# Kernel tuning notes

Measured on AMD Instinct MI355X. Metric: run time of the kernel, lower is better.

The kernel has to match this reference:

```python
import jax, jax.numpy as jnp
import numpy as np

B, S = 2, 2048
D_MODEL, N_HEAD = 2048, 16
D_K = D_MODEL // N_HEAD        # 128
D_C, D_CQ = 512, 1024
D_ROPE = 64
D_NOPE = D_K - D_ROPE          # 64
EPS = 1.1920929e-07            # torch.finfo(float32).eps (nn.RMSNorm default)


def rms_norm(x, w):
    var = jnp.mean(x * x, axis=-1, keepdims=True)
    return x * jax.lax.rsqrt(var + EPS) * w


def setup_inputs() -> dict:
    key = jax.random.key(0)
    ks = jax.random.split(key, 16)
    g = lambda k, shape: (jax.random.normal(k, shape, dtype=jnp.float32) * 0.02)
    return {
        "x": jax.random.normal(ks[0], (B, S, D_MODEL), dtype=jnp.float32),
        "q_down_w": g(ks[1], (D_CQ, D_MODEL)),
        "q_down_b": g(ks[2], (D_CQ,)),
        "q_norm_w": jnp.ones((D_CQ,), jnp.float32),
        "q_up_w": g(ks[3], (N_HEAD * D_K, D_CQ)),
        "q_up_b": g(ks[4], (N_HEAD * D_K,)),
        "kv_down_w": g(ks[5], (D_C, D_MODEL)),
        "kv_down_b": g(ks[6], (D_C,)),
        "kv_norm_w": jnp.ones((D_C,), jnp.float32),
        "kv_up_w": g(ks[7], (N_HEAD * (D_NOPE + D_K), D_C)),
        "kv_up_b": g(ks[8], (N_HEAD * (D_NOPE + D_K),)),
        "k_rope_w": g(ks[9], (N_HEAD * D_ROPE, D_MODEL)),
        "k_rope_b": g(ks[10], (N_HEAD * D_ROPE,)),
        "out_w": g(ks[11], (D_MODEL, D_MODEL)),
        "out_b": g(ks[12], (D_MODEL,)),
    }


def reference(x, q_down_w, q_down_b, q_norm_w, q_up_w, q_up_b,
              kv_down_w, kv_down_b, kv_norm_w, kv_up_w, kv_up_b,
              k_rope_w, k_rope_b, out_w, out_b):
    b, s, _ = x.shape
    # Q low-rank path: down -> RMSNorm -> up
    c_q = rms_norm(x @ q_down_w.T + q_down_b, q_norm_w)              # [b,s,d_cq]
    q = (c_q @ q_up_w.T + q_up_b).reshape(b, s, N_HEAD, D_K)
    q = jnp.transpose(q, (0, 2, 1, 3))                               # [b,h,s,d_k]
    q_nope, q_rope = q[..., :D_NOPE], q[..., D_NOPE:]
    # KV low-rank path
    c_kv = rms_norm(x @ kv_down_w.T + kv_down_b, kv_norm_w)          # [b,s,d_c]
    kv = (c_kv @ kv_up_w.T + kv_up_b).reshape(b, s, N_HEAD, D_NOPE + D_K)
    kv = jnp.transpose(kv, (0, 2, 1, 3))                             # [b,h,s,d_nope+d_k]
    k_nope, v = kv[..., :D_NOPE], kv[..., D_NOPE:]
    # decoupled rope subspace (rope=None config: no rotation applied)
    k_rope = (x @ k_rope_w.T + k_rope_b).reshape(b, s, N_HEAD, D_ROPE)
    k_rope = jnp.transpose(k_rope, (0, 2, 1, 3))                     # [b,h,s,d_rope]
    q = jnp.concatenate([q_nope, q_rope], axis=-1)                   # [b,h,s,d_k]
    k = jnp.concatenate([k_nope, k_rope], axis=-1)                   # [b,h,s,d_k]
    # causal attention
    scores = jnp.einsum('bhnd,bhmd->bhnm', q, k) / np.sqrt(D_K).astype(np.float32)
    mask = jnp.tril(jnp.ones((s, s), dtype=bool))
    scores = jnp.where(mask, scores, -jnp.inf)
    probs = jax.nn.softmax(scores, axis=-1)
    attn = jnp.einsum('bhnm,bhmd->bhnd', probs, v)                   # [b,h,s,d_k]
    attn = jnp.transpose(attn, (0, 2, 1, 3)).reshape(b, s, D_MODEL)
    return attn @ out_w.T + out_b
```

## Files before the change

kernel.cpp:

```cpp
#include <hip/hip_runtime.h>
#include <hip/hip_bf16.h>

typedef __attribute__((ext_vector_type(8))) short bf16x8;
typedef __attribute__((ext_vector_type(4))) float f32x4;
typedef unsigned short u16;

#define RMS_EPS 1.1920929e-07f

constexpr int Bb = 2, Ss = 2048, DM = 2048, NH = 16;
constexpr int MROWS = Bb * Ss;

__device__ __forceinline__ u16 f2bf(float f) {
    __hip_bfloat16 h = __float2bfloat16(f);
    return *reinterpret_cast<u16*>(&h);
}

__device__ __forceinline__ float exp2_fast(float x) {
    float r; asm("v_exp_f32 %0, %1" : "=v"(r) : "v"(x)); return r;
}

__device__ __forceinline__ void gload16(const void* g, void* l) {
    __builtin_amdgcn_global_load_lds(
        (const __attribute__((address_space(1))) unsigned int*)g,
        (__attribute__((address_space(3))) unsigned int*)l, 16, 0, 0);
}

__global__ __launch_bounds__(256) void cvt_all(
    const float* __restrict__ s0, u16* __restrict__ d0,
    const float* __restrict__ s1, u16* __restrict__ d1,
    const float* __restrict__ s2, u16* __restrict__ d2,
    const float* __restrict__ s3, u16* __restrict__ d3,
    const float* __restrict__ s4, u16* __restrict__ d4,
    const float* __restrict__ s5, u16* __restrict__ d5,
    const float* __restrict__ s6, u16* __restrict__ d6)
{
    int i = blockIdx.x * 256 + threadIdx.x;
    const float* s; u16* d; int off;
    if (i < 2097152)      { s = s0; d = d0; off = 0; }
    else if (i < 2621440) { s = s1; d = d1; off = 2097152; }
    else if (i < 2883584) { s = s2; d = d2; off = 2621440; }
    else if (i < 3407872) { s = s3; d = d3; off = 2883584; }
    else if (i < 3932160) { s = s4; d = d4; off = 3407872; }
    else if (i < 4325376) { s = s5; d = d5; off = 3932160; }
    else                  { s = s6; d = d6; off = 4325376; }
    int j = i - off;
    float4 v = reinterpret_cast<const float4*>(s)[j];
    ushort4 o;
    o.x = f2bf(v.x); o.y = f2bf(v.y); o.z = f2bf(v.z); o.w = f2bf(v.w);
    reinterpret_cast<ushort4*>(d)[j] = o;
}

__global__ void build_bcat(const float* __restrict__ qb, const float* __restrict__ kvb,
                           const float* __restrict__ krb, float* __restrict__ bcat) {
    int i = blockIdx.x * 256 + threadIdx.x;
    if (i < 1024) bcat[i] = qb[i];
    else if (i < 1536) bcat[i] = kvb[i - 1024];
    else if (i < 2560) bcat[i] = krb[i - 1536];
}

template <typename OutT>
__global__ __launch_bounds__(256) void gemm_bt(
    const u16* __restrict__ A, const u16* __restrict__ Bt,
    const float* __restrict__ bias, OutT* __restrict__ C,
    int M, int N, int K)
{
    __shared__ alignas(16) u16 sA[128 * 32];
    __shared__ alignas(16) u16 sB[128 * 32];
    const int tid = threadIdx.x;
    const int lane = tid & 63;
    const int w = tid >> 6;
    const int wr = w >> 1, wc = w & 1;
    const int l16 = lane & 15, lq = lane >> 4;
    const int tileM = blockIdx.y * 128;
    const int tileN = blockIdx.x * 128;

    f32x4 acc[4][4];
#pragma unroll
    for (int m = 0; m < 4; m++)
#pragma unroll
        for (int n = 0; n < 4; n++)
#pragma unroll
            for (int r = 0; r < 4; r++) acc[m][n][r] = 0.f;

    const int srow = w * 16 + (lane >> 2);
    const int scol = (lane & 3) * 8;
    const u16* gA0 = A + (size_t)(tileM + srow) * K + scol;
    const u16* gA1 = A + (size_t)(tileM + srow + 64) * K + scol;
    const u16* gB0 = Bt + (size_t)(tileN + srow) * K + scol;
    const u16* gB1 = Bt + (size_t)(tileN + srow + 64) * K + scol;
    u16* lA0 = sA + w * 512;
    u16* lA1 = sA + 2048 + w * 512;
    u16* lB0 = sB + w * 512;
    u16* lB1 = sB + 2048 + w * 512;

    int aoff[4], boff[4];
#pragma unroll
    for (int m = 0; m < 4; m++) aoff[m] = (wr * 64 + m * 16 + l16) * 32 + lq * 8;
#pragma unroll
    for (int n = 0; n < 4; n++) boff[n] = (wc * 64 + n * 16 + l16) * 32 + lq * 8;

    const int nk = K >> 5;
    for (int kk = 0; kk < nk; ++kk) {
        __syncthreads();
        gload16(gA0, lA0);
        gload16(gA1, lA1);
        gload16(gB0, lB0);
        gload16(gB1, lB1);
        gA0 += 32; gA1 += 32; gB0 += 32; gB1 += 32;
        __syncthreads();
        bf16x8 af[4], bfr[4];
#pragma unroll
        for (int m = 0; m < 4; m++) af[m] = *(const bf16x8*)&sA[aoff[m]];
#pragma unroll
        for (int n = 0; n < 4; n++) bfr[n] = *(const bf16x8*)&sB[boff[n]];
        __builtin_amdgcn_s_setprio(1);
#pragma unroll
        for (int m = 0; m < 4; m++)
#pragma unroll
            for (int n = 0; n < 4; n++)
                acc[m][n] = __builtin_amdgcn_mfma_f32_16x16x32_bf16(af[m], bfr[n], acc[m][n], 0, 0, 0);
        __builtin_amdgcn_s_setprio(0);
    }

#pragma unroll
    for (int n = 0; n < 4; n++) {
        int col = tileN + wc * 64 + n * 16 + l16;
        float bv = bias ? bias[col] : 0.f;
#pragma unroll
        for (int m = 0; m < 4; m++) {
            int rowb = tileM + wr * 64 + m * 16 + (lq << 2);
#pragma unroll
            for (int r = 0; r < 4; r++) {
                float v = acc[m][n][r] + bv;
                if constexpr (sizeof(OutT) == 2)
                    C[(size_t)(rowb + r) * N + col] = (OutT)f2bf(v);
                else
                    C[(size_t)(rowb + r) * N + col] = (OutT)v;
            }
        }
    }
}

__global__ __launch_bounds__(256) void gemm_down(
    const u16* __restrict__ A, const u16* __restrict__ Bt,
    const float* __restrict__ bcat, float* __restrict__ dcat,
    u16* __restrict__ krbuf)
{
    constexpr int K = 2048;
    __shared__ alignas(16) u16 sA[128 * 32];
    __shared__ alignas(16) u16 sB[128 * 32];
    const int tid = threadIdx.x;
    const int lane = tid & 63;
    const int w = tid >> 6;
    const int wr = w >> 1, wc = w & 1;
    const int l16 = lane & 15, lq = lane >> 4;
    const int tileM = blockIdx.y * 128;
    const int tileN = blockIdx.x * 128;

    f32x4 acc[4][4];
#pragma unroll
    for (int m = 0; m < 4; m++)
#pragma unroll
        for (int n = 0; n < 4; n++)
#pragma unroll
            for (int r = 0; r < 4; r++) acc[m][n][r] = 0.f;

    const int srow = w * 16 + (lane >> 2);
    const int scol = (lane & 3) * 8;
    const u16* gA0 = A + (size_t)(tileM + srow) * K + scol;
    const u16* gA1 = A + (size_t)(tileM + srow + 64) * K + scol;
    const u16* gB0 = Bt + (size_t)(tileN + srow) * K + scol;
    const u16* gB1 = Bt + (size_t)(tileN + srow + 64) * K + scol;
    u16* lA0 = sA + w * 512;
    u16* lA1 = sA + 2048 + w * 512;
    u16* lB0 = sB + w * 512;
    u16* lB1 = sB + 2048 + w * 512;

    int aoff[4], boff[4];
#pragma unroll
    for (int m = 0; m < 4; m++) aoff[m] = (wr * 64 + m * 16 + l16) * 32 + lq * 8;
#pragma unroll
    for (int n = 0; n < 4; n++) boff[n] = (wc * 64 + n * 16 + l16) * 32 + lq * 8;

    const int nk = K >> 5;
    for (int kk = 0; kk < nk; ++kk) {
        __syncthreads();
        gload16(gA0, lA0);
        gload16(gA1, lA1);
        gload16(gB0, lB0);
        gload16(gB1, lB1);
        gA0 += 32; gA1 += 32; gB0 += 32; gB1 += 32;
        __syncthreads();
        bf16x8 af[4], bfr[4];
#pragma unroll
        for (int m = 0; m < 4; m++) af[m] = *(const bf16x8*)&sA[aoff[m]];
#pragma unroll
        for (int n = 0; n < 4; n++) bfr[n] = *(const bf16x8*)&sB[boff[n]];
        __builtin_amdgcn_s_setprio(1);
#pragma unroll
        for (int m = 0; m < 4; m++)
#pragma unroll
            for (int n = 0; n < 4; n++)
                acc[m][n] = __builtin_amdgcn_mfma_f32_16x16x32_bf16(af[m], bfr[n], acc[m][n], 0, 0, 0);
        __builtin_amdgcn_s_setprio(0);
    }

    const bool isrope = (tileN >= 1536);
#pragma unroll
    for (int n = 0; n < 4; n++) {
        int col = tileN + wc * 64 + n * 16 + l16;
        float bv = bcat[col];
#pragma unroll
        for (int m = 0; m < 4; m++) {
            int rowb = tileM + wr * 64 + m * 16 + (lq << 2);
#pragma unroll
            for (int r = 0; r < 4; r++) {
                float v = acc[m][n][r] + bv;
                if (!isrope) dcat[(size_t)(rowb + r) * 1536 + col] = v;
                else         krbuf[(size_t)(rowb + r) * 1024 + (col - 1536)] = f2bf(v);
            }
        }
    }
}

template <int C>
__global__ __launch_bounds__(256) void rmsnorm_bf16(
    const float* __restrict__ in, int istride, const float* __restrict__ wgt, u16* __restrict__ out)
{
    const int row = blockIdx.x;
    const int tid = threadIdx.x;
    constexpr int PER = C / 256;
    const float* p = in + (size_t)row * istride;
    float v[PER];
    float ss = 0.f;
#pragma unroll
    for (int i = 0; i < PER; i++) { v[i] = p[tid + i * 256]; ss += v[i] * v[i]; }
#pragma unroll
    for (int o = 32; o; o >>= 1) ss += __shfl_xor(ss, o, 64);
    __shared__ float red[4];
    if ((tid & 63) == 0) red[tid >> 6] = ss;
    __syncthreads();
    float tot = red[0] + red[1] + red[2] + red[3];
    float inv = rsqrtf(tot / (float)C + RMS_EPS);
    u16* q = out + (size_t)row * C;
#pragma unroll
    for (int i = 0; i < PER; i++) {
        int c = tid + i * 256;
        q[c] = f2bf(v[i] * inv * wgt[c]);
    }
}

__global__ __launch_bounds__(256) void transpose_v(
    const u16* __restrict__ kvbuf, u16* __restrict__ vT)
{
    __shared__ alignas(16) u16 tile[64][72];
    const int tid = threadIdx.x;
    const int t0 = blockIdx.x * 64;
    const int h = blockIdx.y >> 1, dh = blockIdx.y & 1;
    const int trow = tid >> 2, c8 = (tid & 3) * 8;
    const u16* src = kvbuf + (size_t)(t0 + trow) * 3072 + h * 192 + 64 + dh * 64 + c8;
    *(bf16x8*)&tile[trow][c8]      = *(const bf16x8*)src;
    *(bf16x8*)&tile[trow][c8 + 32] = *(const bf16x8*)(src + 32);
    __syncthreads();
    const int drow = tid >> 2, tc8 = (tid & 3) * 8;
    bf16x8 a, b2;
#pragma unroll
    for (int j = 0; j < 8; j++) {
        a[j]  = (short)tile[tc8 + j][drow];
        b2[j] = (short)tile[tc8 + 32 + j][drow];
    }
    u16* dst = vT + (size_t)(h * 128 + dh * 64 + drow) * MROWS + t0 + tc8;
    *(bf16x8*)dst = a;
    *(bf16x8*)(dst + 32) = b2;
}

__global__ __launch_bounds__(256) void mla_attn(
    const u16* __restrict__ qbuf,
    const u16* __restrict__ kvbuf,
    const u16* __restrict__ krbuf,
    const u16* __restrict__ vT,
    u16* __restrict__ obuf)
{
    const int bh = blockIdx.x;
    const int yy = blockIdx.y;
    const int ii = yy & 7, jj = yy >> 3;
    const int qt = (jj == 0) ? (ii * 2) : (jj == 1) ? (31 - ii * 2)
                 : (jj == 2) ? (ii * 2 + 1) : (30 - ii * 2);
    const int b = bh >> 4, h = bh & 15;
    const int tid = threadIdx.x, lane = tid & 63, w = tid >> 6;
    const int l16 = lane & 15, lq = lane >> 4;

    __shared__ alignas(16) u16 sK[64 * 128];
    __shared__ alignas(16) u16 sVt[128 * 64];
    __shared__ alignas(16) u16 sPT[4][16 * 64];

    const int rowbase = b * Ss;
    const int q0 = qt * 64;
    char* pbase = (char*)sPT[w];

    const int sr = tid >> 2, sc = (tid & 3) * 32;
    const int vd = tid >> 1, vh = (tid & 1) * 32;
    const float C1 = 0.12751742f;
    const float THRR = 90.5f;

    bf16x8 qf[4];
    {
        const u16* qp = qbuf + (size_t)(rowbase + q0 + w * 16 + l16) * 2048 + h * 128 + lq * 8;
#pragma unroll
        for (int c = 0; c < 4; c++) qf[c] = *(const bf16x8*)(qp + c * 32);
    }
    float mi = -3e38f, li = 0.f;
    f32x4 o[8];
#pragma unroll
    for (int d = 0; d < 8; d++)
#pragma unroll
        for (int r = 0; r < 4; r++) o[d][r] = 0.f;

    bf16x8 kr[4], vr[4];
    {
        const int krow = rowbase + sr;
        const u16* src = (sc < 64)
            ? kvbuf + (size_t)krow * 3072 + h * 192 + sc
            : krbuf + (size_t)krow * 1024 + h * 64 + (sc - 64);
#pragma unroll
        for (int j = 0; j < 4; j++) kr[j] = *(const bf16x8*)(src + j * 8);
        const u16* vsrc = vT + (size_t)(h * 128 + vd) * MROWS + rowbase + vh;
#pragma unroll
        for (int j = 0; j < 4; j++) vr[j] = *(const bf16x8*)(vsrc + j * 8);
    }

    for (int kt = 0; kt <= qt; ++kt) {
        __syncthreads();
#pragma unroll
        for (int j = 0; j < 4; j++) {
            int byteoff = sr * 256 + (sc + j * 8) * 2;
            *(bf16x8*)((char*)sK + (byteoff ^ ((sr & 7) << 4))) = kr[j];
        }
#pragma unroll
        for (int j = 0; j < 4; j++) {
            int byteoff = vd * 128 + (vh + j * 8) * 2;
            *(bf16x8*)((char*)sVt + (byteoff ^ ((vd & 7) << 4))) = vr[j];
        }
        __syncthreads();
        if (kt < qt) {
            const int krow = rowbase + (kt + 1) * 64 + sr;
            const u16* src = (sc < 64)
                ? kvbuf + (size_t)krow * 3072 + h * 192 + sc
                : krbuf + (size_t)krow * 1024 + h * 64 + (sc - 64);
#pragma unroll
            for (int j = 0; j < 4; j++) kr[j] = *(const bf16x8*)(src + j * 8);
            const u16* vsrc = vT + (size_t)(h * 128 + vd) * MROWS + rowbase + (kt + 1) * 64 + vh;
#pragma unroll
            for (int j = 0; j < 4; j++) vr[j] = *(const bf16x8*)(vsrc + j * 8);
        }

        f32x4 scf[4];
#pragma unroll
        for (int n = 0; n < 4; n++)
#pragma unroll
            for (int r = 0; r < 4; r++) scf[n][r] = 0.f;
        __builtin_amdgcn_s_setprio(1);
#pragma unroll
        for (int n = 0; n < 4; n++) {
#pragma unroll
            for (int c = 0; c < 4; c++) {
                int row = n * 16 + l16;
                int byteoff = row * 256 + (c * 32 + lq * 8) * 2;
                bf16x8 kf = *(const bf16x8*)((char*)sK + (byteoff ^ ((row & 7) << 4)));
                scf[n] = __builtin_amdgcn_mfma_f32_16x16x32_bf16(kf, qf[c], scf[n], 0, 0, 0);
            }
        }
        __builtin_amdgcn_s_setprio(0);

        if (kt == qt) {
            const int qg = w * 16 + l16;
#pragma unroll
            for (int n = 0; n < 4; n++)
#pragma unroll
                for (int r = 0; r < 4; r++) {
                    int kg = n * 16 + lq * 4 + r;
                    if (kg > qg) scf[n][r] = -3e38f;
                }
        }
        float mx = mi;
#pragma unroll
        for (int n = 0; n < 4; n++)
#pragma unroll
            for (int r = 0; r < 4; r++) mx = fmaxf(mx, scf[n][r]);
        mx = fmaxf(mx, __shfl_xor(mx, 16, 64));
        mx = fmaxf(mx, __shfl_xor(mx, 32, 64));
        if (!__all(mx - mi <= THRR)) {
            float f = exp2_fast((mi - mx) * C1);
            li *= f;
#pragma unroll
            for (int d = 0; d < 8; d++)
#pragma unroll
                for (int r = 0; r < 4; r++) o[d][r] *= f;
            mi = mx;
        }
        float mc = mi * C1;
        float rs = 0.f;
#pragma unroll
        for (int n = 0; n < 4; n++)
#pragma unroll
            for (int r = 0; r < 4; r++) {
                float pv = exp2_fast(__fmaf_rn(scf[n][r], C1, -mc));
                scf[n][r] = pv;
                rs += pv;
            }
        rs += __shfl_xor(rs, 16, 64);
        rs += __shfl_xor(rs, 32, 64);
        li += rs;

#pragma unroll
        for (int n = 0; n < 4; n++) {
            ushort4 pk;
            pk.x = f2bf(scf[n][0]); pk.y = f2bf(scf[n][1]);
            pk.z = f2bf(scf[n][2]); pk.w = f2bf(scf[n][3]);
            int byteoff = l16 * 128 + n * 32 + lq * 8;
            *(ushort4*)(pbase + (byteoff ^ ((l16 & 7) << 4))) = pk;
        }
        __builtin_amdgcn_s_setprio(1);
#pragma unroll
        for (int c = 0; c < 2; c++) {
            int pbyte = l16 * 128 + (c * 32 + lq * 8) * 2;
            bf16x8 pf = *(const bf16x8*)(pbase + (pbyte ^ ((l16 & 7) << 4)));
#pragma unroll
            for (int d = 0; d < 8; d++) {
                int vrow = d * 16 + l16;
                int vbyte = vrow * 128 + (c * 32 + lq * 8) * 2;
                bf16x8 vf = *(const bf16x8*)((char*)sVt + (vbyte ^ ((vrow & 7) << 4)));
                o[d] = __builtin_amdgcn_mfma_f32_16x16x32_bf16(vf, pf, o[d], 0, 0, 0);
            }
        }
        __builtin_amdgcn_s_setprio(0);
    }
    float invl = 1.f / li;
    u16* op = obuf + (size_t)(rowbase + q0 + w * 16 + l16) * 2048 + h * 128;
#pragma unroll
    for (int d = 0; d < 8; d++) {
        ushort4 ok;
        ok.x = f2bf(o[d][0] * invl); ok.y = f2bf(o[d][1] * invl);
        ok.z = f2bf(o[d][2] * invl); ok.w = f2bf(o[d][3] * invl);
        *(ushort4*)(op + d * 16 + lq * 4) = ok;
    }
}

extern "C" void kernel_launch(void* const* d_in, const int* in_sizes, int n_in,
                              void* d_out, int out_size, void* d_ws, size_t ws_size,
                              hipStream_t stream) {
    const float* x        = (const float*)d_in[0];
    const float* q_down_w = (const float*)d_in[1];
    const float* q_down_b = (const float*)d_in[2];
    const float* q_norm_w = (const float*)d_in[3];
    const float* q_up_w   = (const float*)d_in[4];
    const float* q_up_b   = (const float*)d_in[5];
    const float* kv_down_w= (const float*)d_in[6];
    const float* kv_down_b= (const float*)d_in[7];
    const float* kv_norm_w= (const float*)d_in[8];
    const float* kv_up_w  = (const float*)d_in[9];
    const float* kv_up_b  = (const float*)d_in[10];
    const float* k_rope_w = (const float*)d_in[11];
    const float* k_rope_b = (const float*)d_in[12];
    const float* out_w    = (const float*)d_in[13];
    const float* out_b    = (const float*)d_in[14];

    char* ws = (char*)d_ws;
    u16* xbf    = (u16*)(ws + 0);
    u16* wcat   = (u16*)(ws + 16777216);
    u16* quw    = (u16*)(ws + 27262976);
    u16* kvuw   = (u16*)(ws + 31457280);
    u16* outw   = (u16*)(ws + 34603008);
    float* bcat = (float*)(ws + 42991616);
    float* dcat = (float*)(ws + 43008000);
    u16* cq     = (u16*)(ws + 68173824);
    u16* ckv    = (u16*)(ws + 76562432);
    u16* qbuf   = (u16*)(ws + 80756736);
    u16* kvbuf  = (u16*)(ws + 97533952);
    u16* krbuf  = (u16*)(ws + 122699776);
    u16* vT     = (u16*)(ws + 0);
    u16* attnbuf= (u16*)(ws + 43008000);

    cvt_all<<<20992, 256, 0, stream>>>(
        x, xbf,
        q_down_w,  wcat,
        kv_down_w, wcat + 1024 * 2048,
        k_rope_w,  wcat + 1536 * 2048,
        q_up_w,    quw,
        kv_up_w,   kvuw,
        out_w,     outw);
    build_bcat<<<10, 256, 0, stream>>>(q_down_b, kv_down_b, k_rope_b, bcat);

    gemm_down<<<dim3(20, 32), 256, 0, stream>>>(xbf, wcat, bcat, dcat, krbuf);
    rmsnorm_bf16<1024><<<MROWS, 256, 0, stream>>>(dcat, 1536, q_norm_w, cq);
    rmsnorm_bf16<512><<<MROWS, 256, 0, stream>>>(dcat + 1024, 1536, kv_norm_w, ckv);
    gemm_bt<u16><<<dim3(16, 32), 256, 0, stream>>>(cq, quw, q_up_b, qbuf, MROWS, 2048, 1024);
    gemm_bt<u16><<<dim3(24, 32), 256, 0, stream>>>(ckv, kvuw, kv_up_b, kvbuf, MROWS, 3072, 512);
    transpose_v<<<dim3(64, 32), 256, 0, stream>>>(kvbuf, vT);
    mla_attn<<<dim3(32, 32), 256, 0, stream>>>(qbuf, kvbuf, krbuf, vT, attnbuf);
    gemm_bt<float><<<dim3(16, 32), 256, 0, stream>>>(attnbuf, outw, out_b, (float*)d_out, MROWS, 2048, 2048);
}
```

Measured before the change: 285.4 us.

## Rework attention to 128-row query tiles with 32x32 MFMA and register P

Attention blocks now cover 128 query rows, with each wave owning 32 rows. Scores and PV products use 32x32x16 bf16 MFMAs, and P is exchanged through lane shuffles instead of an LDS staging buffer. This halves the number of blocks and doubles K/V reuse per LDS load, and waves whose rows are fully masked skip compute. The GEMM kernels also get an XCD-aware block remap to improve L2 locality, and launch bounds request two blocks per CU for attention. The trade-off is higher register pressure and fewer blocks for load balance.

```diff
diff --git a/kernel.cpp b/kernel.cpp
--- a/kernel.cpp
+++ b/kernel.cpp
@@ -3,7 +3,9 @@
 
 typedef __attribute__((ext_vector_type(8))) short bf16x8;
 typedef __attribute__((ext_vector_type(4))) float f32x4;
+typedef __attribute__((ext_vector_type(16))) float f32x16;
 typedef unsigned short u16;
+typedef unsigned int u32;
 
 #define RMS_EPS 1.1920929e-07f
 
@@ -58,6 +60,17 @@
     else if (i < 2560) bcat[i] = krb[i - 1536];
 }
 
+__device__ __forceinline__ void xcd_remap(int& bx, int& by) {
+    int nx = gridDim.x, ny = gridDim.y;
+    int nwg = nx * ny;
+    if ((nwg & 7) != 0) return;
+    int flat = blockIdx.x + nx * blockIdx.y;
+    int chunk = nwg >> 3;
+    int wg = (flat & 7) * chunk + (flat >> 3);
+    by = wg % ny;
+    bx = wg / ny;
+}
+
 template <typename OutT>
 __global__ __launch_bounds__(256) void gemm_bt(
     const u16* __restrict__ A, const u16* __restrict__ Bt,
@@ -71,8 +84,10 @@
     const int w = tid >> 6;
     const int wr = w >> 1, wc = w & 1;
     const int l16 = lane & 15, lq = lane >> 4;
-    const int tileM = blockIdx.y * 128;
-    const int tileN = blockIdx.x * 128;
+    int bx = blockIdx.x, by = blockIdx.y;
+    xcd_remap(bx, by);
+    const int tileM = by * 128;
+    const int tileN = bx * 128;
 
     f32x4 acc[4][4];
 #pragma unroll
@@ -154,8 +169,10 @@
     const int w = tid >> 6;
     const int wr = w >> 1, wc = w & 1;
     const int l16 = lane & 15, lq = lane >> 4;
-    const int tileM = blockIdx.y * 128;
-    const int tileN = blockIdx.x * 128;
+    int bx = blockIdx.x, by = blockIdx.y;
+    xcd_remap(bx, by);
+    const int tileM = by * 128;
+    const int tileN = bx * 128;
 
     f32x4 acc[4][4];
 #pragma unroll
@@ -274,7 +291,7 @@
     *(bf16x8*)(dst + 32) = b2;
 }
 
-__global__ __launch_bounds__(256) void mla_attn(
+__global__ __launch_bounds__(256, 2) void mla_attn(
     const u16* __restrict__ qbuf,
     const u16* __restrict__ kvbuf,
     const u16* __restrict__ krbuf,
@@ -282,54 +299,53 @@
     u16* __restrict__ obuf)
 {
     const int bh = blockIdx.x;
-    const int yy = blockIdx.y;
-    const int ii = yy & 7, jj = yy >> 3;
-    const int qt = (jj == 0) ? (ii * 2) : (jj == 1) ? (31 - ii * 2)
-                 : (jj == 2) ? (ii * 2 + 1) : (30 - ii * 2);
-    const int b = bh >> 4, h = bh & 15;
+    const int y = blockIdx.y;
+    const int ii = y & 7, jj = y >> 3;
+    const int qt = jj ? (15 - 2 * ii) : (2 * ii);
+    const int b = bh >> 4, hh = bh & 15;
     const int tid = threadIdx.x, lane = tid & 63, w = tid >> 6;
-    const int l16 = lane & 15, lq = lane >> 4;
+    const int l31 = lane & 31, hx = lane >> 5;
 
     __shared__ alignas(16) u16 sK[64 * 128];
     __shared__ alignas(16) u16 sVt[128 * 64];
-    __shared__ alignas(16) u16 sPT[4][16 * 64];
 
     const int rowbase = b * Ss;
-    const int q0 = qt * 64;
-    char* pbase = (char*)sPT[w];
+    const int q0 = qt * 128;
+    const int nkt = 2 * qt + 2;
 
     const int sr = tid >> 2, sc = (tid & 3) * 32;
     const int vd = tid >> 1, vh = (tid & 1) * 32;
     const float C1 = 0.12751742f;
     const float THRR = 90.5f;
 
-    bf16x8 qf[4];
+    bf16x8 qf[8];
     {
-        const u16* qp = qbuf + (size_t)(rowbase + q0 + w * 16 + l16) * 2048 + h * 128 + lq * 8;
-#pragma unroll
-        for (int c = 0; c < 4; c++) qf[c] = *(const bf16x8*)(qp + c * 32);
+        const u16* qp = qbuf + (size_t)(rowbase + q0 + w * 32 + l31) * 2048 + hh * 128;
+#pragma unroll
+        for (int c = 0; c < 8; c++) qf[c] = *(const bf16x8*)(qp + (2 * c + hx) * 8);
     }
     float mi = -3e38f, li = 0.f;
-    f32x4 o[8];
-#pragma unroll
-    for (int d = 0; d < 8; d++)
-#pragma unroll
-        for (int r = 0; r < 4; r++) o[d][r] = 0.f;
+    f32x16 o[4];
+#pragma unroll
+    for (int d = 0; d < 4; d++)
+#pragma unroll
+        for (int i = 0; i < 16; i++) o[d][i] = 0.f;
 
     bf16x8 kr[4], vr[4];
     {
         const int krow = rowbase + sr;
         const u16* src = (sc < 64)
-            ? kvbuf + (size_t)krow * 3072 + h * 192 + sc
-            : krbuf + (size_t)krow * 1024 + h * 64 + (sc - 64);
+            ? kvbuf + (size_t)krow * 3072 + hh * 192 + sc
+            : krbuf + (size_t)krow * 1024 + hh * 64 + (sc - 64);
 #pragma unroll
         for (int j = 0; j < 4; j++) kr[j] = *(const bf16x8*)(src + j * 8);
-        const u16* vsrc = vT + (size_t)(h * 128 + vd) * MROWS + rowbase + vh;
+        const u16* vsrc = vT + (size_t)(hh * 128 + vd) * MROWS + rowbase + vh;
 #pragma unroll
         for (int j = 0; j < 4; j++) vr[j] = *(const bf16x8*)(vsrc + j * 8);
     }
 
-    for (int kt = 0; kt <= qt; ++kt) {
+#pragma unroll 1
+    for (int kt = 0; kt < nkt; ++kt) {
         __syncthreads();
 #pragma unroll
         for (int j = 0; j < 4; j++) {
@@ -342,108 +358,123 @@
             *(bf16x8*)((char*)sVt + (byteoff ^ ((vd & 7) << 4))) = vr[j];
         }
         __syncthreads();
-        if (kt < qt) {
+        if (kt + 1 < nkt) {
             const int krow = rowbase + (kt + 1) * 64 + sr;
             const u16* src = (sc < 64)
-                ? kvbuf + (size_t)krow * 3072 + h * 192 + sc
-                : krbuf + (size_t)krow * 1024 + h * 64 + (sc - 64);
+                ? kvbuf + (size_t)krow * 3072 + hh * 192 + sc
+                : krbuf + (size_t)krow * 1024 + hh * 64 + (sc - 64);
 #pragma unroll
             for (int j = 0; j < 4; j++) kr[j] = *(const bf16x8*)(src + j * 8);
-            const u16* vsrc = vT + (size_t)(h * 128 + vd) * MROWS + rowbase + (kt + 1) * 64 + vh;
+            const u16* vsrc = vT + (size_t)(hh * 128 + vd) * MROWS + rowbase + (kt + 1) * 64 + vh;
 #pragma unroll
             for (int j = 0; j < 4; j++) vr[j] = *(const bf16x8*)(vsrc + j * 8);
         }
 
-        f32x4 scf[4];
-#pragma unroll
-        for (int n = 0; n < 4; n++)
-#pragma unroll
-            for (int r = 0; r < 4; r++) scf[n][r] = 0.f;
-        __builtin_amdgcn_s_setprio(1);
-#pragma unroll
-        for (int n = 0; n < 4; n++) {
-#pragma unroll
-            for (int c = 0; c < 4; c++) {
-                int row = n * 16 + l16;
-                int byteoff = row * 256 + (c * 32 + lq * 8) * 2;
-                bf16x8 kf = *(const bf16x8*)((char*)sK + (byteoff ^ ((row & 7) << 4)));
-                scf[n] = __builtin_amdgcn_mfma_f32_16x16x32_bf16(kf, qf[c], scf[n], 0, 0, 0);
+        const bool alive = (kt * 64) <= (q0 + w * 32 + 31);
+        if (alive) {
+            f32x16 scf[2];
+#pragma unroll
+            for (int b2 = 0; b2 < 2; b2++)
+#pragma unroll
+                for (int i = 0; i < 16; i++) scf[b2][i] = 0.f;
+            __builtin_amdgcn_s_setprio(1);
+#pragma unroll
+            for (int s = 0; s < 8; s++) {
+#pragma unroll
+                for (int b2 = 0; b2 < 2; b2++) {
+                    int krow = b2 * 32 + l31;
+                    int kbyte = (krow * 256 + s * 32 + hx * 16) ^ ((l31 & 7) << 4);
+                    bf16x8 kf = *(const bf16x8*)((char*)sK + kbyte);
+                    scf[b2] = __builtin_amdgcn_mfma_f32_32x32x16_bf16(kf, qf[s], scf[b2], 0, 0, 0);
+                }
             }
-        }
-        __builtin_amdgcn_s_setprio(0);
-
-        if (kt == qt) {
-            const int qg = w * 16 + l16;
-#pragma unroll
-            for (int n = 0; n < 4; n++)
-#pragma unroll
-                for (int r = 0; r < 4; r++) {
-                    int kg = n * 16 + lq * 4 + r;
-                    if (kg > qg) scf[n][r] = -3e38f;
+            __builtin_amdgcn_s_setprio(0);
+
+            if (kt * 64 + 63 > q0 + w * 32) {
+                const int qg = q0 + w * 32 + l31;
+#pragma unroll
+                for (int b2 = 0; b2 < 2; b2++)
+#pragma unroll
+                    for (int rg = 0; rg < 16; rg++) {
+                        int kg = kt * 64 + b2 * 32 + (rg & 3) + 8 * (rg >> 2) + 4 * hx;
+                        if (kg > qg) scf[b2][rg] = -3e38f;
+                    }
+            }
+            float mx = mi;
+#pragma unroll
+            for (int b2 = 0; b2 < 2; b2++)
+#pragma unroll
+                for (int rg = 0; rg < 16; rg++) mx = fmaxf(mx, scf[b2][rg]);
+            mx = fmaxf(mx, __shfl_xor(mx, 32, 64));
+            if (!__all(mx - mi <= THRR)) {
+                float f = exp2_fast((mi - mx) * C1);
+                li *= f;
+#pragma unroll
+                for (int d = 0; d < 4; d++)
+#pragma unroll
+                    for (int i = 0; i < 16; i++) o[d][i] *= f;
+                mi = mx;
+            }
+            float mc = mi * C1;
+            float rs = 0.f;
+#pragma unroll
+            for (int b2 = 0; b2 < 2; b2++)
+#pragma unroll
+                for (int rg = 0; rg < 16; rg++) {
+                    float pv = exp2_fast(__fmaf_rn(scf[b2][rg], C1, -mc));
+                    scf[b2][rg] = pv;
+                    rs += pv;
                 }
-        }
-        float mx = mi;
-#pragma unroll
-        for (int n = 0; n < 4; n++)
-#pragma unroll
-            for (int r = 0; r < 4; r++) mx = fmaxf(mx, scf[n][r]);
-        mx = fmaxf(mx, __shfl_xor(mx, 16, 64));
-        mx = fmaxf(mx, __shfl_xor(mx, 32, 64));
-        if (!__all(mx - mi <= THRR)) {
-            float f = exp2_fast((mi - mx) * C1);
-            li *= f;
-#pragma unroll
-            for (int d = 0; d < 8; d++)
-#pragma unroll
-                for (int r = 0; r < 4; r++) o[d][r] *= f;
-            mi = mx;
-        }
-        float mc = mi * C1;
-        float rs = 0.f;
-#pragma unroll
-        for (int n = 0; n < 4; n++)
-#pragma unroll
-            for (int r = 0; r < 4; r++) {
-                float pv = exp2_fast(__fmaf_rn(scf[n][r], C1, -mc));
-                scf[n][r] = pv;
-                rs += pv;
+            rs += __shfl_xor(rs, 32, 64);
+            li += rs;
+
+            u32 pk[2][4][2];
+#pragma unroll
+            for (int b2 = 0; b2 < 2; b2++)
+#pragma unroll
+                for (int g = 0; g < 4; g++) {
+                    pk[b2][g][0] = (u32)f2bf(scf[b2][4 * g + 0]) | ((u32)f2bf(scf[b2][4 * g + 1]) << 16);
+                    pk[b2][g][1] = (u32)f2bf(scf[b2][4 * g + 2]) | ((u32)f2bf(scf[b2][4 * g + 3]) << 16);
+                }
+
+            __builtin_amdgcn_s_setprio(1);
+#pragma unroll
+            for (int t = 0; t < 4; t++) {
+                const int b2 = t >> 1, s = t & 1;
+                u32 send0 = hx ? pk[b2][2 * s][0] : pk[b2][2 * s + 1][0];
+                u32 send1 = hx ? pk[b2][2 * s][1] : pk[b2][2 * s + 1][1];
+                u32 r0 = (u32)__shfl_xor((int)send0, 32, 64);
+                u32 r1 = (u32)__shfl_xor((int)send1, 32, 64);
+                union { u32 wd[4]; bf16x8 v; } pu;
+                pu.wd[0] = hx ? r0 : pk[b2][2 * s][0];
+                pu.wd[1] = hx ? r1 : pk[b2][2 * s][1];
+                pu.wd[2] = hx ? pk[b2][2 * s + 1][0] : r0;
+                pu.wd[3] = hx ? pk[b2][2 * s + 1][1] : r1;
+#pragma unroll
+                for (int dblk = 0; dblk < 4; dblk++) {
+                    int vrow = dblk * 32 + l31;
+                    int vbyte = (vrow * 128 + t * 32 + hx * 16) ^ ((l31 & 7) << 4);
+                    bf16x8 vf = *(const bf16x8*)((char*)sVt + vbyte);
+                    o[dblk] = __builtin_amdgcn_mfma_f32_32x32x16_bf16(vf, pu.v, o[dblk], 0, 0, 0);
+                }
             }
-        rs += __shfl_xor(rs, 16, 64);
-        rs += __shfl_xor(rs, 32, 64);
-        li += rs;
-
-#pragma unroll
-        for (int n = 0; n < 4; n++) {
-            ushort4 pk;
-            pk.x = f2bf(scf[n][0]); pk.y = f2bf(scf[n][1]);
-            pk.z = f2bf(scf[n][2]); pk.w = f2bf(scf[n][3]);
-            int byteoff = l16 * 128 + n * 32 + lq * 8;
-            *(ushort4*)(pbase + (byteoff ^ ((l16 & 7) << 4))) = pk;
-        }
-        __builtin_amdgcn_s_setprio(1);
-#pragma unroll
-        for (int c = 0; c < 2; c++) {
-            int pbyte = l16 * 128 + (c * 32 + lq * 8) * 2;
-            bf16x8 pf = *(const bf16x8*)(pbase + (pbyte ^ ((l16 & 7) << 4)));
-#pragma unroll
-            for (int d = 0; d < 8; d++) {
-                int vrow = d * 16 + l16;
-                int vbyte = vrow * 128 + (c * 32 + lq * 8) * 2;
-                bf16x8 vf = *(const bf16x8*)((char*)sVt + (vbyte ^ ((vrow & 7) << 4)));
-                o[d] = __builtin_amdgcn_mfma_f32_16x16x32_bf16(vf, pf, o[d], 0, 0, 0);
-            }
-        }
-        __builtin_amdgcn_s_setprio(0);
+            __builtin_amdgcn_s_setprio(0);
+        }
     }
     float invl = 1.f / li;
-    u16* op = obuf + (size_t)(rowbase + q0 + w * 16 + l16) * 2048 + h * 128;
-#pragma unroll
-    for (int d = 0; d < 8; d++) {
-        ushort4 ok;
-        ok.x = f2bf(o[d][0] * invl); ok.y = f2bf(o[d][1] * invl);
-        ok.z = f2bf(o[d][2] * invl); ok.w = f2bf(o[d][3] * invl);
-        *(ushort4*)(op + d * 16 + lq * 4) = ok;
-    }
+    u16* op = obuf + (size_t)(rowbase + q0 + w * 32 + l31) * 2048 + hh * 128;
+#pragma unroll
+    for (int dblk = 0; dblk < 4; dblk++)
+#pragma unroll
+        for (int rg = 0; rg < 4; rg++) {
+            int d0 = dblk * 32 + rg * 8 + hx * 4;
+            ushort4 ov;
+            ov.x = f2bf(o[dblk][rg * 4 + 0] * invl);
+            ov.y = f2bf(o[dblk][rg * 4 + 1] * invl);
+            ov.z = f2bf(o[dblk][rg * 4 + 2] * invl);
+            ov.w = f2bf(o[dblk][rg * 4 + 3] * invl);
+            *(ushort4*)(op + d0) = ov;
+        }
 }
 
 extern "C" void kernel_launch(void* const* d_in, const int* in_sizes, int n_in,
@@ -497,6 +528,6 @@
     gemm_bt<u16><<<dim3(16, 32), 256, 0, stream>>>(cq, quw, q_up_b, qbuf, MROWS, 2048, 1024);
     gemm_bt<u16><<<dim3(24, 32), 256, 0, stream>>>(ckv, kvuw, kv_up_b, kvbuf, MROWS, 3072, 512);
     transpose_v<<<dim3(64, 32), 256, 0, stream>>>(kvbuf, vT);
-    mla_attn<<<dim3(32, 32), 256, 0, stream>>>(qbuf, kvbuf, krbuf, vT, attnbuf);
+    mla_attn<<<dim3(32, 16), 256, 0, stream>>>(qbuf, kvbuf, krbuf, vT, attnbuf);
     gemm_bt<float><<<dim3(16, 32), 256, 0, stream>>>(attnbuf, outw, out_b, (float*)d_out, MROWS, 2048, 2048);
 }
```

Result: faster. 266.8 us (-6.5%).
